# Kernel optimization log

Hardware: AMD Instinct MI355X
Metric: run time of the kernel (lower is better)

Reference implementation:

```python
import jax, jax.numpy as jnp
import numpy as np

RAD = 4   # corr lookup radius
NH, NP = 8, 4  # deform attn heads / points (single level)


def conv2d(x, w, b, pad):
    y = jax.lax.conv_general_dilated(x, w, (1, 1), [(pad, pad), (pad, pad)],
                                     dimension_numbers=('NCHW', 'OIHW', 'NCHW'))
    return y + b[None, :, None, None]


def bilinear_gather(imgf, H, W, px, py):
    # imgf: [N, C, H*W]; px, py: [N, P] pixel coords; zero padding (grid_sample 'zeros')
    x0 = jnp.floor(px); y0 = jnp.floor(py)
    wx = px - x0; wy = py - y0
    def tap(xi, yi, wt):
        valid = (xi >= 0) & (xi <= W - 1) & (yi >= 0) & (yi <= H - 1)
        idx = (jnp.clip(yi, 0, H - 1) * W + jnp.clip(xi, 0, W - 1)).astype(jnp.int32)
        v = jnp.take_along_axis(imgf, idx[:, None, :], axis=2)
        return v * (wt * valid)[:, None, :]
    return (tap(x0, y0, (1 - wx) * (1 - wy)) + tap(x0 + 1, y0, wx * (1 - wy))
            + tap(x0, y0 + 1, (1 - wx) * wy) + tap(x0 + 1, y0 + 1, wx * wy))


def sine_pos_embed(B, H, W, npf, temperature=10000.0):
    # PositionEmbeddingSine with normalize=True
    scale = 2.0 * np.pi; eps = 1e-6
    y = jnp.broadcast_to(jnp.arange(1, H + 1, dtype=jnp.float32)[:, None], (H, W))
    x = jnp.broadcast_to(jnp.arange(1, W + 1, dtype=jnp.float32)[None, :], (H, W))
    y = (y - 0.5) / (H + eps) * scale
    x = (x - 0.5) / (W + eps) * scale
    dim_t = temperature ** (2.0 * (jnp.arange(npf) // 2).astype(jnp.float32) / npf)
    px = x[..., None] / dim_t
    py = y[..., None] / dim_t
    px = jnp.stack([jnp.sin(px[..., 0::2]), jnp.cos(px[..., 1::2])], -1).reshape(H, W, npf)
    py = jnp.stack([jnp.sin(py[..., 0::2]), jnp.cos(py[..., 1::2])], -1).reshape(H, W, npf)
    pos = jnp.concatenate([py, px], -1)
    return jnp.broadcast_to(pos[None], (B, H, W, 2 * npf)).reshape(B, H * W, 2 * npf)


def layer_norm(x, g, b):
    m = x.mean(-1, keepdims=True)
    v = ((x - m) ** 2).mean(-1, keepdims=True)
    return (x - m) / jnp.sqrt(v + 1e-5) * g + b


def _forward(fmap1, fmap2, flow, wc1, bc1, wc2, bc2, wf1, bf1, wf2, bf2, wcf, bcf,
             wfh1, bfh1, wfh2, bfh2, w_off, b_off, w_aw, b_aw, w_val, b_val,
             w_out, b_out, ln1_g, ln1_b, w_ff1, b_ff1, w_ff2, b_ff2, ln2_g, ln2_b):
    B, C, H, W = fmap1.shape
    HW = H * W
    dh = C // NH
    relu = jax.nn.relu
    # ---- CorrBlock.corr: all-pairs correlation volume ----
    corr = jnp.einsum('bcq,bck->bqk', fmap1.reshape(B, C, HW), fmap2.reshape(B, C, HW))
    corr = corr / jnp.sqrt(jnp.asarray(C, jnp.float32))
    corrf = corr.reshape(B * HW, 1, HW)  # [B*HW, 1, H2*W2]
    # ---- correlation lookup at coords = base grid + flow (bilinear, align_corners=True) ----
    gy, gx = jnp.meshgrid(jnp.arange(H, dtype=jnp.float32),
                          jnp.arange(W, dtype=jnp.float32), indexing='ij')
    cx = (gx[None] + flow[:, 0]).reshape(B * HW)
    cy = (gy[None] + flow[:, 1]).reshape(B * HW)
    d = jnp.linspace(-RAD, RAD, 2 * RAD + 1)
    oy, ox = jnp.meshgrid(d, d, indexing='ij')  # RAFT quirk: delta[...,0]=dy, delta[...,1]=dx
    px = cx[:, None] + oy.reshape(-1)[None, :]
    py = cy[:, None] + ox.reshape(-1)[None, :]
    corr_feat = bilinear_gather(corrf, H, W, px, py).reshape(B, H, W, (2 * RAD + 1) ** 2)
    corr_feat = corr_feat.transpose(0, 3, 1, 2)  # [B, 81, H, W]
    # ---- BasicMotionEncoder + FlowHead (BasicUpdateBlock.forward path) ----
    cor = relu(conv2d(corr_feat, wc1, bc1, 0))
    cor = relu(conv2d(cor, wc2, bc2, 1))
    flo = relu(conv2d(flow, wf1, bf1, 3))
    flo = relu(conv2d(flo, wf2, bf2, 1))
    mf = relu(conv2d(jnp.concatenate([cor, flo], 1), wcf, bcf, 1))
    mf = jnp.concatenate([mf, flow], 1)  # [B,128,H,W]
    delta_flow = conv2d(relu(conv2d(mf, wfh1, bfh1, 1)), wfh2, bfh2, 1)  # [B,2,H,W]
    # ---- single-level MSDeformAttn encoder layer over fmap1 tokens ----
    src = fmap1.reshape(B, C, HW).transpose(0, 2, 1)  # [B, Lq, C]
    pos = sine_pos_embed(B, H, W, C // 2)
    q = src + pos
    off = (q @ w_off.T + b_off).reshape(B, HW, NH, 1, NP, 2)
    aw = jax.nn.softmax((q @ w_aw.T + b_aw).reshape(B, HW, NH, NP), axis=-1)
    val = (src @ w_val.T + b_val).reshape(B, HW, NH, dh)
    ref = jnp.stack([(gx.reshape(-1) + 0.5) / W, (gy.reshape(-1) + 0.5) / H], -1)  # [HW,2]
    loc = (ref[None, :, None, None, None, :] + off / jnp.asarray([W, H], jnp.float32))[:, :, :, 0]
    # normalized loc -> pixel coords with align_corners=False convention
    px2 = (loc[..., 0] * W - 0.5).transpose(0, 2, 1, 3).reshape(B * NH, HW * NP)
    py2 = (loc[..., 1] * H - 0.5).transpose(0, 2, 1, 3).reshape(B * NH, HW * NP)
    vflat = val.transpose(0, 2, 3, 1).reshape(B * NH, dh, HW)
    samp = bilinear_gather(vflat, H, W, px2, py2).reshape(B, NH, dh, HW, NP)
    attn = (samp * aw.transpose(0, 2, 1, 3)[:, :, None]).sum(-1)  # [B,NH,dh,HW]
    attn = attn.transpose(0, 3, 1, 2).reshape(B, HW, C) @ w_out.T + b_out
    src = layer_norm(src + attn, ln1_g, ln1_b)
    ff = jax.nn.relu(src @ w_ff1.T + b_ff1) @ w_ff2.T + b_ff2
    src = layer_norm(src + ff, ln2_g, ln2_b)
    return src, delta_flow


def setup_inputs():
    key = jax.random.key(0)
    ks = jax.random.split(key, 20)
    B, C, H, W = 4, 256, 48, 48
    def w(i, shape, s=0.02):
        return jax.random.normal(ks[i], shape, jnp.float32) * s
    return {
        'fmap1': jax.random.normal(ks[0], (B, C, H, W), jnp.float32),
        'fmap2': jax.random.normal(ks[1], (B, C, H, W), jnp.float32),
        'flow': jax.random.normal(ks[2], (B, 2, H, W), jnp.float32),
        'wc1': w(3, (256, 81, 1, 1)), 'bc1': jnp.zeros((256,)),
        'wc2': w(4, (192, 256, 3, 3)), 'bc2': jnp.zeros((192,)),
        'wf1': w(5, (128, 2, 7, 7)), 'bf1': jnp.zeros((128,)),
        'wf2': w(6, (64, 128, 3, 3)), 'bf2': jnp.zeros((64,)),
        'wcf': w(7, (126, 256, 3, 3)), 'bcf': jnp.zeros((126,)),
        'wfh1': w(8, (256, 128, 3, 3)), 'bfh1': jnp.zeros((256,)),
        'wfh2': w(9, (2, 256, 3, 3)), 'bfh2': jnp.zeros((2,)),
        'w_off': w(10, (64, 256)), 'b_off': jnp.zeros((64,)),
        'w_aw': w(11, (32, 256)), 'b_aw': jnp.zeros((32,)),
        'w_val': w(12, (256, 256)), 'b_val': jnp.zeros((256,)),
        'w_out': w(13, (256, 256)), 'b_out': jnp.zeros((256,)),
        'ln1_g': jnp.ones((256,)), 'ln1_b': jnp.zeros((256,)),
        'w_ff1': w(14, (1024, 256)), 'b_ff1': jnp.zeros((1024,)),
        'w_ff2': w(15, (256, 1024)), 'b_ff2': jnp.zeros((256,)),
        'ln2_g': jnp.ones((256,)), 'ln2_b': jnp.zeros((256,)),
    }


def reference(fmap1, fmap2, flow, wc1, bc1, wc2, bc2, wf1, bf1, wf2, bf2, wcf, bcf,
              wfh1, bfh1, wfh2, bfh2, w_off, b_off, w_aw, b_aw, w_val, b_val,
              w_out, b_out, ln1_g, ln1_b, w_ff1, b_ff1, w_ff2, b_ff2, ln2_g, ln2_b):
    return _forward(fmap1, fmap2, flow, wc1, bc1, wc2, bc2, wf1, bf1, wf2, bf2, wcf, bcf,
                    wfh1, bfh1, wfh2, bfh2, w_off, b_off, w_aw, b_aw, w_val, b_val,
                    w_out, b_out, ln1_g, ln1_b, w_ff1, b_ff1, w_ff2, b_ff2, ln2_g, ln2_b)
```

## Files before the change

kernel.cpp:

```cpp
#include <hip/hip_runtime.h>
#include <hip/hip_bf16.h>
#include <math.h>

#define HH 48
#define WW 48
#define HW 2304
#define BB 4
#define CC 256

typedef __hip_bfloat16 bf16;
typedef __attribute__((ext_vector_type(8))) short s8v;
typedef __attribute__((ext_vector_type(4))) float f4v;

__device__ inline float bf2f(short u) {
  unsigned v = ((unsigned)(unsigned short)u) << 16;
  return __builtin_bit_cast(float, v);
}

__global__ __launch_bounds__(256) void prep_k(const float* __restrict__ fmap1,
                                              const float* __restrict__ fmap2,
                                              float* __restrict__ srcT,
                                              bf16* __restrict__ f1t,
                                              bf16* __restrict__ qb,
                                              bf16* __restrict__ f2t) {
  __shared__ float t[64][65];
  int z = blockIdx.z;
  int p0 = blockIdx.x * 64, c0 = blockIdx.y * 64;
  int b = z & 3;
  const float* src = (z < 4) ? fmap2 : fmap1;
  const float* inb = src + ((size_t)b * CC + c0) * HW + p0;
#pragma unroll
  for (int i = 0; i < 16; ++i) {
    int idx = threadIdx.x + i * 256;
    int c = idx >> 6, p = idx & 63;
    t[c][p] = inb[(size_t)c * HW + p];
  }
  __syncthreads();
  if (z < 4) {
    bf16* ob = f2t + ((size_t)b * HW + p0) * 256 + c0;
#pragma unroll
    for (int i = 0; i < 16; ++i) {
      int idx = threadIdx.x + i * 256;
      int p = idx >> 6, c = idx & 63;
      ob[(size_t)p * 256 + c] = (bf16)t[c][p];
    }
  } else {
    const float TWO_PI = 6.283185307179586f;
#pragma unroll
    for (int i = 0; i < 16; ++i) {
      int idx = threadIdx.x + i * 256;
      int pl = idx >> 6, cl = idx & 63;
      int c = c0 + cl;
      int p = p0 + pl;
      int y = p / WW, x = p % WW;
      float s = t[cl][pl];
      int axis = c >> 7;
      int cc = c & 127;
      int mm = cc >> 1;
      float coord = (axis ? ((float)x + 0.5f) : ((float)y + 0.5f)) * (TWO_PI / (48.f + 1e-6f));
      float tp = exp2f((float)mm * (13.287712379549449f / 64.f));
      float a = coord / tp;
      float pv = (cc & 1) ? cosf(a) : sinf(a);
      size_t o = ((size_t)b * HW + p) * 256 + c;
      srcT[o] = s;
      f1t[o] = (bf16)s;
      qb[o] = (bf16)(s + pv);
    }
  }
}

__global__ __launch_bounds__(256) void corr_mfma_k(const bf16* __restrict__ f1t,
                                                   const bf16* __restrict__ f2t,
                                                   bf16* __restrict__ corr) {
  int b = blockIdx.z;
  int m0 = blockIdx.y * 128, n0 = blockIdx.x * 64;
  __shared__ short As[2][128][64];
  __shared__ short Bs[2][64][64];
  int tid = threadIdx.x;
  int arl = tid >> 1, asl = (tid & 1) * 4;
  int brl = tid >> 2, bsl = (tid & 3) * 2;
  int wave = tid >> 6, lane = tid & 63;
  int wm = (wave >> 1) * 64, wn = (wave & 1) * 32;
  int fl = lane & 15, fk8 = lane >> 4;
  f4v acc[4][2] = {};
  const bf16* arow = f1t + ((size_t)b * HW + m0 + arl) * 256;
  const bf16* brow = f2t + ((size_t)b * HW + n0 + brl) * 256;
  uint4 apre[4], bpre[2];
#pragma unroll
  for (int q = 0; q < 4; ++q) apre[q] = *(const uint4*)(arow + (asl + q) * 8);
#pragma unroll
  for (int q = 0; q < 2; ++q) bpre[q] = *(const uint4*)(brow + (bsl + q) * 8);
  int cur = 0;
  for (int st = 0; st < 4; ++st) {
#pragma unroll
    for (int q = 0; q < 4; ++q) {
      int sr = asl + q;
      *(uint4*)&As[cur][arl][((sr ^ (arl & 7))) * 8] = apre[q];
    }
#pragma unroll
    for (int q = 0; q < 2; ++q) {
      int sr = bsl + q;
      *(uint4*)&Bs[cur][brl][((sr ^ (brl & 7))) * 8] = bpre[q];
    }
    if (st < 3) {
      int c0 = (st + 1) * 64;
#pragma unroll
      for (int q = 0; q < 4; ++q) apre[q] = *(const uint4*)(arow + c0 + (asl + q) * 8);
#pragma unroll
      for (int q = 0; q < 2; ++q) bpre[q] = *(const uint4*)(brow + c0 + (bsl + q) * 8);
    }
    __syncthreads();
#pragma unroll
    for (int cc = 0; cc < 2; ++cc) {
      s8v af[4], bfr[2];
#pragma unroll
      for (int i = 0; i < 4; ++i) {
        int ar = wm + i * 16 + fl;
        af[i] = *(const s8v*)&As[cur][ar][(((cc * 4 + fk8) ^ (ar & 7))) * 8];
      }
#pragma unroll
      for (int j = 0; j < 2; ++j) {
        int br = wn + j * 16 + fl;
        bfr[j] = *(const s8v*)&Bs[cur][br][(((cc * 4 + fk8) ^ (br & 7))) * 8];
      }
#pragma unroll
      for (int i = 0; i < 4; ++i)
#pragma unroll
        for (int j = 0; j < 2; ++j)
          acc[i][j] = __builtin_amdgcn_mfma_f32_16x16x32_bf16(af[i], bfr[j], acc[i][j], 0, 0, 0);
    }
    cur ^= 1;
  }
  bf16* outp = corr + ((size_t)b * HW + m0) * HW + n0;
#pragma unroll
  for (int j = 0; j < 2; ++j) {
    int o = wn + j * 16 + fl;
#pragma unroll
    for (int i = 0; i < 4; ++i)
#pragma unroll
      for (int r = 0; r < 4; ++r) {
        int m = wm + i * 16 + fk8 * 4 + r;
        outp[(size_t)m * HW + o] = (bf16)(acc[i][j][r] * 0.0625f);
      }
  }
}

__global__ __launch_bounds__(256) void corr_lookup_k(const bf16* __restrict__ corr,
                                                     const float* __restrict__ flow,
                                                     bf16* __restrict__ cf) {
  int g = blockIdx.x * 256 + threadIdx.x;
  int t = g % 96;
  int n = g / 96;
  if (t >= 81) { cf[g] = (bf16)0.f; return; }
  int b = n / HW;
  int p = n % HW;
  int y = p / WW, x = p % WW;
  float fx = flow[((size_t)b * 2 + 0) * HW + p];
  float fy = flow[((size_t)b * 2 + 1) * HW + p];
  float px = (float)x + fx + (float)(t / 9 - 4);
  float py = (float)y + fy + (float)(t % 9 - 4);
  const bf16* row = corr + (size_t)n * HW;
  float x0f = floorf(px), y0f = floorf(py);
  int x0 = (int)x0f, y0 = (int)y0f;
  float wx = px - x0f, wy = py - y0f;
  float acc = 0.f;
  if ((unsigned)x0 < WW && (unsigned)y0 < HH) acc += (float)row[y0 * WW + x0] * (1.f - wx) * (1.f - wy);
  if ((unsigned)(x0 + 1) < WW && (unsigned)y0 < HH) acc += (float)row[y0 * WW + x0 + 1] * wx * (1.f - wy);
  if ((unsigned)x0 < WW && (unsigned)(y0 + 1) < HH) acc += (float)row[(y0 + 1) * WW + x0] * (1.f - wx) * wy;
  if ((unsigned)(x0 + 1) < WW && (unsigned)(y0 + 1) < HH) acc += (float)row[(y0 + 1) * WW + x0 + 1] * wx * wy;
  cf[g] = (bf16)acc;
}

struct WtSegs {
  const float* src[12];
  unsigned dstOff[12];
  int Cout[12], Cin[12], KP[12], KS2[12];
  unsigned cum[13];
};

__global__ __launch_bounds__(256) void wt_all_k(WtSegs s, bf16* __restrict__ base) {
  unsigned idx = blockIdx.x * 256 + threadIdx.x;
  if (idx >= s.cum[12]) return;
  int seg = 0;
#pragma unroll
  for (int i = 1; i < 12; ++i)
    if (idx >= s.cum[i]) seg = i;
  unsigned r = idx - s.cum[seg];
  int KP = s.KP[seg], Cout = s.Cout[seg], Cin = s.Cin[seg], KS2 = s.KS2[seg];
  int c = r % KP;
  int o = (r / KP) % Cout;
  int t = r / (KP * Cout);
  float v;
  if (KS2 == 0) {
    int cc = c >> 6, tt = c & 63;
    v = (tt < 49) ? s.src[seg][((size_t)o * 2 + cc) * 49 + tt] : 0.f;
  } else {
    v = (c < Cin) ? s.src[seg][((size_t)o * Cin + c) * KS2 + t] : 0.f;
  }
  base[s.dstOff[seg] + r] = (bf16)v;
}

__global__ __launch_bounds__(256) void im2col7_k(const float* __restrict__ flow,
                                                 bf16* __restrict__ col7) {
  int g = blockIdx.x * 256 + threadIdx.x;
  int kp = g & 127;
  int n = g >> 7;
  int b = n / HW;
  int p = n % HW;
  int y = p / WW, x = p % WW;
  int cc = kp >> 6, tt = kp & 63;
  float v = 0.f;
  if (tt < 49) {
    int ky = tt / 7, kx = tt % 7;
    int yy = y + ky - 3, xx = x + kx - 3;
    if ((unsigned)yy < (unsigned)HH && (unsigned)xx < (unsigned)WW)
      v = flow[((size_t)b * 2 + cc) * HW + yy * WW + xx];
  }
  col7[g] = (bf16)v;
}

struct GSegs {
  const bf16* in[4];
  const bf16* wt[4];
  const float* bias[4];
  const float* bias2[4];
  float* outf[4];
  bf16* outb[4];
  int split[4], O[4], KP[4], taps[4], OStride[4], OOff[4], relu[4], nTn[4];
  int blkStart[4];
  int nseg;
};

__global__ __launch_bounds__(256) void gemm_group_k(GSegs s) {
  int blk = blockIdx.x;
  int seg = 0;
#pragma unroll
  for (int i = 1; i < 4; ++i)
    if (i < s.nseg && blk >= s.blkStart[i]) seg = i;
  int rel = blk - s.blkStart[seg];
  int nTn = s.nTn[seg];
  int bm = rel / nTn, bn = rel % nTn;
  int m0 = bm * 128, n0 = bn * 64;
  int KP = s.KP[seg], O = s.O[seg], taps = s.taps[seg];
  const bf16* in = s.in[seg];
  const bf16* wt = s.wt[seg];

  __shared__ short As[2][128][64];
  __shared__ short Bs[2][64][64];
  int tid = threadIdx.x;
  int arl = tid >> 1, asl = (tid & 1) * 4;
  int brl = tid >> 2, bsl = (tid & 3) * 2;
  int wave = tid >> 6, lane = tid & 63;
  int wm = (wave >> 1) * 64, wn = (wave & 1) * 32;
  int fl = lane & 15, fk8 = lane >> 4;
  f4v acc[4][2] = {};
  int m = m0 + arl;
  int b = m / HW;
  int p = m - b * HW;
  int y = p / WW, x = p - y * WW;
  int wo = n0 + brl;
  bool wvalid = wo < O;
  int wo_c = wvalid ? wo : 0;

  int nc0 = (KP + 63) >> 6;
  int S = taps * nc0;
  uint4 apre[4], bpre[2];

  auto load_stage = [&](int st) {
    int t = st / nc0;
    int c0 = (st - t * nc0) * 64;
    int yy = y, xx = x;
    bool valid = true;
    if (taps == 9) {
      int ky = t / 3, kx = t - ky * 3;
      yy = y + ky - 1;
      xx = x + kx - 1;
      valid = ((unsigned)yy < (unsigned)HH) & ((unsigned)xx < (unsigned)WW);
    }
    const bf16* arow = in + ((size_t)b * HW + yy * WW + xx) * KP;
    const bf16* wrow = wt + ((size_t)t * O + wo_c) * KP;
#pragma unroll
    for (int q = 0; q < 4; ++q) {
      int col = c0 + (asl + q) * 8;
      uint4 v = {0u, 0u, 0u, 0u};
      if (valid && col < KP) v = *(const uint4*)(arow + col);
      apre[q] = v;
    }
#pragma unroll
    for (int q = 0; q < 2; ++q) {
      int col = c0 + (bsl + q) * 8;
      uint4 v = {0u, 0u, 0u, 0u};
      if (wvalid && col < KP) v = *(const uint4*)(wrow + col);
      bpre[q] = v;
    }
  };

  load_stage(0);
  int cur = 0;
  for (int st = 0; st < S; ++st) {
#pragma unroll
    for (int q = 0; q < 4; ++q) {
      int sr = asl + q;
      *(uint4*)&As[cur][arl][((sr ^ (arl & 7))) * 8] = apre[q];
    }
#pragma unroll
    for (int q = 0; q < 2; ++q) {
      int sr = bsl + q;
      *(uint4*)&Bs[cur][brl][((sr ^ (brl & 7))) * 8] = bpre[q];
    }
    if (st + 1 < S) load_stage(st + 1);
    __syncthreads();
#pragma unroll
    for (int cc = 0; cc < 2; ++cc) {
      s8v af[4], bfr[2];
#pragma unroll
      for (int i = 0; i < 4; ++i) {
        int ar = wm + i * 16 + fl;
        af[i] = *(const s8v*)&As[cur][ar][(((cc * 4 + fk8) ^ (ar & 7))) * 8];
      }
#pragma unroll
      for (int j = 0; j < 2; ++j) {
        int br = wn + j * 16 + fl;
        bfr[j] = *(const s8v*)&Bs[cur][br][(((cc * 4 + fk8) ^ (br & 7))) * 8];
      }
#pragma unroll
      for (int i = 0; i < 4; ++i)
#pragma unroll
        for (int j = 0; j < 2; ++j)
          acc[i][j] = __builtin_amdgcn_mfma_f32_16x16x32_bf16(af[i], bfr[j], acc[i][j], 0, 0, 0);
    }
    cur ^= 1;
  }
  int OStride = s.OStride[seg], OOff = s.OOff[seg], relu = s.relu[seg], split = s.split[seg];
  const float* bias = s.bias[seg];
  const float* bias2 = s.bias2[seg];
  float* outf = s.outf[seg];
  bf16* outb = s.outb[seg];
#pragma unroll
  for (int j = 0; j < 2; ++j) {
    int o = n0 + wn + j * 16 + fl;
    if (o < O) {
      float bsv = (bias2 != nullptr && o >= split) ? bias2[o - split] : bias[o];
#pragma unroll
      for (int i = 0; i < 4; ++i)
#pragma unroll
        for (int r = 0; r < 4; ++r) {
          int mm = m0 + wm + i * 16 + fk8 * 4 + r;
          float v = acc[i][j][r] + bsv;
          if (relu) v = fmaxf(v, 0.f);
          if (outb) outb[(size_t)mm * OStride + OOff + o] = (bf16)v;
          else outf[(size_t)mm * OStride + OOff + o] = v;
        }
    }
  }
}

__global__ __launch_bounds__(256) void convfh2_k(const bf16* __restrict__ fh1,
                                                 const float* __restrict__ w,
                                                 const float* __restrict__ bias,
                                                 float* __restrict__ out) {
  __shared__ float wl[4608];
  int tid = threadIdx.x;
#pragma unroll
  for (int i = tid; i < 4608; i += 256) {
    int o2 = i & 1;
    int t = (i >> 1) % 9;
    int c = i / 18;
    wl[i] = w[((size_t)o2 * 256 + c) * 9 + t];
  }
  __syncthreads();
  int wave = tid >> 6, lane = tid & 63;
  int pix = blockIdx.x * 4 + wave;
  int b = pix / HW;
  int q = pix % HW;
  int y = q / WW, x = q % WW;
  int c0 = lane * 4;
  float a0 = 0.f, a1 = 0.f;
#pragma unroll
  for (int ky = 0; ky < 3; ++ky) {
    int yy = y + ky - 1;
    if ((unsigned)yy >= (unsigned)HH) continue;
#pragma unroll
    for (int kx = 0; kx < 3; ++kx) {
      int xx = x + kx - 1;
      if ((unsigned)xx >= (unsigned)WW) continue;
      int t = ky * 3 + kx;
      const bf16* row = fh1 + ((size_t)b * HW + yy * WW + xx) * 256 + c0;
      ushort4 v = *(const ushort4*)row;
      unsigned short vv[4] = {v.x, v.y, v.z, v.w};
#pragma unroll
      for (int j = 0; j < 4; ++j) {
        float fv = bf2f((short)vv[j]);
        float2 wp = *(const float2*)&wl[((c0 + j) * 9 + t) * 2];
        a0 += fv * wp.x;
        a1 += fv * wp.y;
      }
    }
  }
#pragma unroll
  for (int offl = 32; offl > 0; offl >>= 1) {
    a0 += __shfl_xor(a0, offl);
    a1 += __shfl_xor(a1, offl);
  }
  if (lane == 0) {
    out[(size_t)b * 2 * HW + q] = a0 + bias[0];
    out[((size_t)b * 2 + 1) * HW + q] = a1 + bias[1];
  }
}

__global__ void copy_flow_k(const float* __restrict__ flow, bf16* __restrict__ mf) {
  int g = blockIdx.x * 256 + threadIdx.x;
  int p = g % HW;
  int c = (g / HW) % 2;
  int b = g / (2 * HW);
  mf[((size_t)b * HW + p) * 128 + 126 + c] = (bf16)flow[g];
}

__global__ __launch_bounds__(256) void deform_k(const float* __restrict__ val,
                                                const float* __restrict__ oa,
                                                bf16* __restrict__ attn) {
  int g = blockIdx.x * 256 + threadIdx.x;
  int d = g & 31;
  int nh = g >> 5;
  int h = nh & 7;
  int n = nh >> 3;
  int b = n / HW;
  int p = n % HW;
  int y = p / WW, x = p % WW;
  const float* ap = oa + (size_t)n * 96 + 64 + h * 4;
  float l0 = ap[0], l1 = ap[1], l2 = ap[2], l3 = ap[3];
  float mx = fmaxf(fmaxf(l0, l1), fmaxf(l2, l3));
  float e0 = expf(l0 - mx), e1 = expf(l1 - mx), e2 = expf(l2 - mx), e3 = expf(l3 - mx);
  float inv = 1.f / (e0 + e1 + e2 + e3);
  float wts[4] = {e0 * inv, e1 * inv, e2 * inv, e3 * inv};
  const float* offp = oa + (size_t)n * 96 + h * 8;
  const float* vb = val + (size_t)b * HW * 256 + h * 32 + d;
  float acc = 0.f;
#pragma unroll
  for (int pt = 0; pt < 4; ++pt) {
    float ox = offp[pt * 2 + 0];
    float oy = offp[pt * 2 + 1];
    float w = wts[pt];
    float px = (float)x + ox, py = (float)y + oy;
    float x0f = floorf(px), y0f = floorf(py);
    int x0 = (int)x0f, y0 = (int)y0f;
    float wx = px - x0f, wy = py - y0f;
    float s = 0.f;
    if ((unsigned)x0 < WW && (unsigned)y0 < HH)
      s += vb[(size_t)(y0 * WW + x0) * 256] * (1.f - wx) * (1.f - wy);
    if ((unsigned)(x0 + 1) < WW && (unsigned)y0 < HH)
      s += vb[(size_t)(y0 * WW + x0 + 1) * 256] * wx * (1.f - wy);
    if ((unsigned)x0 < WW && (unsigned)(y0 + 1) < HH)
      s += vb[(size_t)((y0 + 1) * WW + x0) * 256] * (1.f - wx) * wy;
    if ((unsigned)(x0 + 1) < WW && (unsigned)(y0 + 1) < HH)
      s += vb[(size_t)((y0 + 1) * WW + x0 + 1) * 256] * wx * wy;
    acc += w * s;
  }
  attn[(size_t)n * 256 + h * 32 + d] = (bf16)acc;
}

__global__ __launch_bounds__(256) void ln_add_k(const float* __restrict__ A,
                                                const float* __restrict__ Bv,
                                                const float* __restrict__ g,
                                                const float* __restrict__ be,
                                                float* __restrict__ out,
                                                bf16* __restrict__ outb) {
  int n = blockIdx.x;
  int c = threadIdx.x;
  float v = A[(size_t)n * 256 + c] + Bv[(size_t)n * 256 + c];
  float s1 = v, s2 = v * v;
#pragma unroll
  for (int o = 32; o > 0; o >>= 1) {
    s1 += __shfl_down(s1, o);
    s2 += __shfl_down(s2, o);
  }
  __shared__ float r1[4], r2[4], mv[2];
  int wid = c >> 6, lane = c & 63;
  if (lane == 0) {
    r1[wid] = s1;
    r2[wid] = s2;
  }
  __syncthreads();
  if (c == 0) {
    float a = r1[0] + r1[1] + r1[2] + r1[3];
    float q2 = r2[0] + r2[1] + r2[2] + r2[3];
    float mean = a * (1.f / 256.f);
    mv[0] = mean;
    mv[1] = q2 * (1.f / 256.f) - mean * mean;
  }
  __syncthreads();
  float mean = mv[0], var = mv[1];
  float r = (v - mean) * rsqrtf(var + 1e-5f) * g[c] + be[c];
  out[(size_t)n * 256 + c] = r;
  if (outb) outb[(size_t)n * 256 + c] = (bf16)r;
}

extern "C" void kernel_launch(void* const* d_in, const int* in_sizes, int n_in,
                              void* d_out, int out_size, void* d_ws, size_t ws_size,
                              hipStream_t stream) {
  const float* fmap1 = (const float*)d_in[0];
  const float* fmap2 = (const float*)d_in[1];
  const float* flow = (const float*)d_in[2];
  const float* wc1 = (const float*)d_in[3];
  const float* bc1 = (const float*)d_in[4];
  const float* wc2 = (const float*)d_in[5];
  const float* bc2 = (const float*)d_in[6];
  const float* wf1 = (const float*)d_in[7];
  const float* bf1 = (const float*)d_in[8];
  const float* wf2 = (const float*)d_in[9];
  const float* bf2 = (const float*)d_in[10];
  const float* wcf = (const float*)d_in[11];
  const float* bcf = (const float*)d_in[12];
  const float* wfh1 = (const float*)d_in[13];
  const float* bfh1 = (const float*)d_in[14];
  const float* wfh2 = (const float*)d_in[15];
  const float* bfh2 = (const float*)d_in[16];
  const float* w_off = (const float*)d_in[17];
  const float* b_off = (const float*)d_in[18];
  const float* w_aw = (const float*)d_in[19];
  const float* b_aw = (const float*)d_in[20];
  const float* w_val = (const float*)d_in[21];
  const float* b_val = (const float*)d_in[22];
  const float* w_out = (const float*)d_in[23];
  const float* b_out = (const float*)d_in[24];
  const float* ln1_g = (const float*)d_in[25];
  const float* ln1_b = (const float*)d_in[26];
  const float* w_ff1 = (const float*)d_in[27];
  const float* b_ff1 = (const float*)d_in[28];
  const float* w_ff2 = (const float*)d_in[29];
  const float* b_ff2 = (const float*)d_in[30];
  const float* ln2_g = (const float*)d_in[31];
  const float* ln2_b = (const float*)d_in[32];

  float* ws = (float*)d_ws;
  float* out_src = (float*)d_out;
  float* out_df = out_src + (size_t)BB * HW * CC;

  const size_t F_WT = 0;
  const size_t F_CORR = 1000000;
  const size_t F_F1T = 11700000;
  const size_t F_F2T = 12900000;
  const size_t F_QB = 14100000;
  const size_t F_SRCT = 15300000;
  const size_t F_CF = 17700000;
  const size_t F_COL7 = 18200000;
  const size_t F_COR1 = 18800000;
  const size_t F_FLO1 = 20000000;
  const size_t F_CAT = 20600000;
  const size_t F_MF = 21800000;
  const size_t F_FH1 = 22400000;
  const size_t F_OA = 23600000;
  const size_t F_VAL = 24500000;
  const size_t F_ATTN = 26900000;
  const size_t F_TMP = 28100000;
  const size_t F_SRC1 = 30500000;
  const size_t F_SRC1B = 32900000;
  const size_t F_FF1 = 34100000;
  const size_t F_FF2 = 38900000;

  bf16* wkbase = (bf16*)(ws + F_WT);
  bf16* wk1 = wkbase + 0;
  bf16* wk2 = wkbase + 24576;
  bf16* wkf2 = wkbase + 466944;
  bf16* wkcf = wkbase + 540672;
  bf16* wkfh1 = wkbase + 830976;
  bf16* wl_oa = wkbase + 1125888;
  bf16* wl_val = wkbase + 1150464;
  bf16* wl_out = wkbase + 1216000;
  bf16* wl_ff1 = wkbase + 1281536;
  bf16* wl_ff2 = wkbase + 1543680;
  bf16* wk7 = wkbase + 1805824;
  bf16* corrb = (bf16*)(ws + F_CORR);
  bf16* f1t = (bf16*)(ws + F_F1T);
  bf16* f2t = (bf16*)(ws + F_F2T);
  bf16* qb = (bf16*)(ws + F_QB);
  bf16* cf = (bf16*)(ws + F_CF);
  bf16* col7 = (bf16*)(ws + F_COL7);
  bf16* cor1 = (bf16*)(ws + F_COR1);
  bf16* flo1 = (bf16*)(ws + F_FLO1);
  bf16* cat = (bf16*)(ws + F_CAT);
  bf16* mf = (bf16*)(ws + F_MF);
  bf16* fh1 = (bf16*)(ws + F_FH1);
  bf16* attnb = (bf16*)(ws + F_ATTN);
  bf16* src1b = (bf16*)(ws + F_SRC1B);
  bf16* ff1b = (bf16*)(ws + F_FF1);

  WtSegs segs;
  const float* srcs[12] = {wc1, wc2, wf2, wcf, wfh1, w_off, w_aw, w_val, w_out, w_ff1, w_ff2, wf1};
  unsigned offs[12] = {0, 24576, 466944, 540672, 830976, 1125888, 1142272, 1150464, 1216000, 1281536, 1543680, 1805824};
  int couts[12] = {256, 192, 64, 126, 256, 64, 32, 256, 256, 1024, 256, 128};
  int cins[12] = {81, 256, 128, 256, 128, 256, 256, 256, 256, 256, 1024, 2};
  int kps[12] = {96, 256, 128, 256, 128, 256, 256, 256, 256, 256, 1024, 128};
  int ks2[12] = {1, 9, 9, 9, 9, 1, 1, 1, 1, 1, 1, 0};
  unsigned cum = 0;
  for (int i = 0; i < 12; ++i) {
    segs.src[i] = srcs[i];
    segs.dstOff[i] = offs[i];
    segs.Cout[i] = couts[i];
    segs.Cin[i] = cins[i];
    segs.KP[i] = kps[i];
    segs.KS2[i] = ks2[i];
    segs.cum[i] = cum;
    cum += (unsigned)((ks2[i] ? ks2[i] : 1) * couts[i] * kps[i]);
  }
  segs.cum[12] = cum;
  wt_all_k<<<dim3((cum + 255) / 256), 256, 0, stream>>>(segs, wkbase);

  prep_k<<<dim3(36, 4, 8), 256, 0, stream>>>(fmap1, fmap2, ws + F_SRCT, f1t, qb, f2t);
  im2col7_k<<<dim3(4608), 256, 0, stream>>>(flow, col7);
  copy_flow_k<<<dim3(72), 256, 0, stream>>>(flow, mf);

  corr_mfma_k<<<dim3(36, 18, 4), 256, 0, stream>>>(f1t, f2t, corrb);
  corr_lookup_k<<<dim3(3456), 256, 0, stream>>>(corrb, flow, cf);

  auto setseg = [](GSegs& G, int i, const bf16* in, const bf16* wt, const float* bias,
                   const float* bias2, int split, float* outf, bf16* outb, int O, int KP,
                   int taps, int OStride, int OOff, int relu) {
    G.in[i] = in; G.wt[i] = wt; G.bias[i] = bias; G.bias2[i] = bias2; G.split[i] = split;
    G.outf[i] = outf; G.outb[i] = outb; G.O[i] = O; G.KP[i] = KP; G.taps[i] = taps;
    G.OStride[i] = OStride; G.OOff[i] = OOff; G.relu[i] = relu;
    G.nTn[i] = (O + 63) / 64;
  };
  auto finseg = [](GSegs& G, int n) {
    int cumb = 0;
    for (int i = 0; i < 4; ++i) {
      if (i < n) { G.blkStart[i] = cumb; cumb += G.nTn[i] * 72; }
      else G.blkStart[i] = 0x7fffffff;
    }
    G.nseg = n;
    return cumb;
  };

  GSegs GA;
  setseg(GA, 0, cf, wk1, bc1, nullptr, 1 << 30, nullptr, cor1, 256, 96, 1, 256, 0, 1);
  setseg(GA, 1, col7, wk7, bf1, nullptr, 1 << 30, nullptr, flo1, 128, 128, 1, 128, 0, 1);
  setseg(GA, 2, qb, wl_oa, b_off, b_aw, 64, ws + F_OA, nullptr, 96, 256, 1, 96, 0, 0);
  setseg(GA, 3, f1t, wl_val, b_val, nullptr, 1 << 30, ws + F_VAL, nullptr, 256, 256, 1, 256, 0, 0);
  int nblkA = finseg(GA, 4);
  gemm_group_k<<<dim3(nblkA), 256, 0, stream>>>(GA);

  deform_k<<<dim3(9216), 256, 0, stream>>>(ws + F_VAL, ws + F_OA, attnb);

  GSegs GB;
  setseg(GB, 0, cor1, wk2, bc2, nullptr, 1 << 30, nullptr, cat, 192, 256, 9, 256, 0, 1);
  setseg(GB, 1, flo1, wkf2, bf2, nullptr, 1 << 30, nullptr, cat, 64, 128, 9, 256, 192, 1);
  setseg(GB, 2, attnb, wl_out, b_out, nullptr, 1 << 30, ws + F_TMP, nullptr, 256, 256, 1, 256, 0, 0);
  int nblkB = finseg(GB, 3);
  gemm_group_k<<<dim3(nblkB), 256, 0, stream>>>(GB);

  ln_add_k<<<dim3(9216), 256, 0, stream>>>(ws + F_TMP, ws + F_SRCT, ln1_g, ln1_b, ws + F_SRC1, src1b);

  GSegs GC;
  setseg(GC, 0, cat, wkcf, bcf, nullptr, 1 << 30, nullptr, mf, 126, 256, 9, 128, 0, 1);
  setseg(GC, 1, src1b, wl_ff1, b_ff1, nullptr, 1 << 30, nullptr, ff1b, 1024, 256, 1, 1024, 0, 1);
  int nblkC = finseg(GC, 2);
  gemm_group_k<<<dim3(nblkC), 256, 0, stream>>>(GC);

  GSegs GD;
  setseg(GD, 0, mf, wkfh1, bfh1, nullptr, 1 << 30, nullptr, fh1, 256, 128, 9, 256, 0, 1);
  setseg(GD, 1, ff1b, wl_ff2, b_ff2, nullptr, 1 << 30, ws + F_FF2, nullptr, 256, 1024, 1, 256, 0, 0);
  int nblkD = finseg(GD, 2);
  gemm_group_k<<<dim3(nblkD), 256, 0, stream>>>(GD);

  convfh2_k<<<dim3(2304), 256, 0, stream>>>(fh1, wfh2, bfh2, out_df);
  ln_add_k<<<dim3(9216), 256, 0, stream>>>(ws + F_FF2, ws + F_SRC1, ln2_g, ln2_b, out_src, nullptr);

  (void)in_sizes; (void)n_in; (void)out_size; (void)ws_size;
}
```

Baseline: 286.0 us.

## Fuse correlation and lookup into local-window dot products per pixel

Replaces the all-pairs MFMA correlation volume and the separate bilinear lookup kernel with one kernel. For each pixel it computes dot products only for the 10x10 integer window around the flow target, then bilinearly interpolates the 9x9 taps from that shared window. The goal is to skip the full HWxHW matmul and the large bf16 correlation buffer write and read. In exchange the dot products run as scalar FMAs with gathered f2t rows instead of on matrix cores, and corr values are no longer rounded to bf16 before interpolation.

```diff
diff --git a/kernel.cpp b/kernel.cpp
--- a/kernel.cpp
+++ b/kernel.cpp
@@ -69,106 +69,71 @@
   }
 }
 
-__global__ __launch_bounds__(256) void corr_mfma_k(const bf16* __restrict__ f1t,
-                                                   const bf16* __restrict__ f2t,
-                                                   bf16* __restrict__ corr) {
-  int b = blockIdx.z;
-  int m0 = blockIdx.y * 128, n0 = blockIdx.x * 64;
-  __shared__ short As[2][128][64];
-  __shared__ short Bs[2][64][64];
-  int tid = threadIdx.x;
-  int arl = tid >> 1, asl = (tid & 1) * 4;
-  int brl = tid >> 2, bsl = (tid & 3) * 2;
-  int wave = tid >> 6, lane = tid & 63;
-  int wm = (wave >> 1) * 64, wn = (wave & 1) * 32;
-  int fl = lane & 15, fk8 = lane >> 4;
-  f4v acc[4][2] = {};
-  const bf16* arow = f1t + ((size_t)b * HW + m0 + arl) * 256;
-  const bf16* brow = f2t + ((size_t)b * HW + n0 + brl) * 256;
-  uint4 apre[4], bpre[2];
-#pragma unroll
-  for (int q = 0; q < 4; ++q) apre[q] = *(const uint4*)(arow + (asl + q) * 8);
-#pragma unroll
-  for (int q = 0; q < 2; ++q) bpre[q] = *(const uint4*)(brow + (bsl + q) * 8);
-  int cur = 0;
-  for (int st = 0; st < 4; ++st) {
-#pragma unroll
-    for (int q = 0; q < 4; ++q) {
-      int sr = asl + q;
-      *(uint4*)&As[cur][arl][((sr ^ (arl & 7))) * 8] = apre[q];
-    }
-#pragma unroll
-    for (int q = 0; q < 2; ++q) {
-      int sr = bsl + q;
-      *(uint4*)&Bs[cur][brl][((sr ^ (brl & 7))) * 8] = bpre[q];
-    }
-    if (st < 3) {
-      int c0 = (st + 1) * 64;
-#pragma unroll
-      for (int q = 0; q < 4; ++q) apre[q] = *(const uint4*)(arow + c0 + (asl + q) * 8);
-#pragma unroll
-      for (int q = 0; q < 2; ++q) bpre[q] = *(const uint4*)(brow + c0 + (bsl + q) * 8);
-    }
-    __syncthreads();
-#pragma unroll
-    for (int cc = 0; cc < 2; ++cc) {
-      s8v af[4], bfr[2];
-#pragma unroll
-      for (int i = 0; i < 4; ++i) {
-        int ar = wm + i * 16 + fl;
-        af[i] = *(const s8v*)&As[cur][ar][(((cc * 4 + fk8) ^ (ar & 7))) * 8];
-      }
-#pragma unroll
-      for (int j = 0; j < 2; ++j) {
-        int br = wn + j * 16 + fl;
-        bfr[j] = *(const s8v*)&Bs[cur][br][(((cc * 4 + fk8) ^ (br & 7))) * 8];
-      }
-#pragma unroll
-      for (int i = 0; i < 4; ++i)
-#pragma unroll
-        for (int j = 0; j < 2; ++j)
-          acc[i][j] = __builtin_amdgcn_mfma_f32_16x16x32_bf16(af[i], bfr[j], acc[i][j], 0, 0, 0);
-    }
-    cur ^= 1;
-  }
-  bf16* outp = corr + ((size_t)b * HW + m0) * HW + n0;
-#pragma unroll
-  for (int j = 0; j < 2; ++j) {
-    int o = wn + j * 16 + fl;
-#pragma unroll
-    for (int i = 0; i < 4; ++i)
-#pragma unroll
-      for (int r = 0; r < 4; ++r) {
-        int m = wm + i * 16 + fk8 * 4 + r;
-        outp[(size_t)m * HW + o] = (bf16)(acc[i][j][r] * 0.0625f);
-      }
-  }
-}
-
-__global__ __launch_bounds__(256) void corr_lookup_k(const bf16* __restrict__ corr,
-                                                     const float* __restrict__ flow,
-                                                     bf16* __restrict__ cf) {
-  int g = blockIdx.x * 256 + threadIdx.x;
-  int t = g % 96;
-  int n = g / 96;
-  if (t >= 81) { cf[g] = (bf16)0.f; return; }
-  int b = n / HW;
-  int p = n % HW;
-  int y = p / WW, x = p % WW;
+__global__ __launch_bounds__(256) void fused_corr_k(const bf16* __restrict__ f1t,
+                                                    const bf16* __restrict__ f2t,
+                                                    const float* __restrict__ flow,
+                                                    bf16* __restrict__ cf) {
+  __shared__ float f1s[4][260];
+  __shared__ float Dls[4][112];
+  int wave = threadIdx.x >> 6, lane = threadIdx.x & 63;
+  int q = blockIdx.x * 4 + wave;
+  int b = q / HW, p = q - b * HW;
+  int y = p / WW, x = p - y * WW;
+  {
+    ushort4 v = *(const ushort4*)(f1t + (size_t)q * 256 + lane * 4);
+    f1s[wave][lane * 4 + 0] = bf2f((short)v.x);
+    f1s[wave][lane * 4 + 1] = bf2f((short)v.y);
+    f1s[wave][lane * 4 + 2] = bf2f((short)v.z);
+    f1s[wave][lane * 4 + 3] = bf2f((short)v.w);
+  }
   float fx = flow[((size_t)b * 2 + 0) * HW + p];
   float fy = flow[((size_t)b * 2 + 1) * HW + p];
-  float px = (float)x + fx + (float)(t / 9 - 4);
-  float py = (float)y + fy + (float)(t % 9 - 4);
-  const bf16* row = corr + (size_t)n * HW;
-  float x0f = floorf(px), y0f = floorf(py);
-  int x0 = (int)x0f, y0 = (int)y0f;
-  float wx = px - x0f, wy = py - y0f;
-  float acc = 0.f;
-  if ((unsigned)x0 < WW && (unsigned)y0 < HH) acc += (float)row[y0 * WW + x0] * (1.f - wx) * (1.f - wy);
-  if ((unsigned)(x0 + 1) < WW && (unsigned)y0 < HH) acc += (float)row[y0 * WW + x0 + 1] * wx * (1.f - wy);
-  if ((unsigned)x0 < WW && (unsigned)(y0 + 1) < HH) acc += (float)row[(y0 + 1) * WW + x0] * (1.f - wx) * wy;
-  if ((unsigned)(x0 + 1) < WW && (unsigned)(y0 + 1) < HH) acc += (float)row[(y0 + 1) * WW + x0 + 1] * wx * wy;
-  cf[g] = (bf16)acc;
+  float sx = (float)x + fx, sy = (float)y + fy;
+  float fx0 = floorf(sx), fy0 = floorf(sy);
+  int ix0 = (int)fx0, iy0 = (int)fy0;
+  float wx = sx - fx0, wy = sy - fy0;
+  __syncthreads();
+  const float* f1p = f1s[wave];
+#pragma unroll
+  for (int r = 0; r < 2; ++r) {
+    int idx = lane + r * 64;
+    if (idx < 100) {
+      int jy = idx / 10, jx = idx - jy * 10;
+      int ky = iy0 - 4 + jy, kx = ix0 - 4 + jx;
+      float acc = 0.f;
+      if ((unsigned)kx < (unsigned)WW && (unsigned)ky < (unsigned)HH) {
+        const bf16* row = f2t + ((size_t)b * HW + ky * WW + kx) * 256;
+#pragma unroll
+        for (int c8 = 0; c8 < 32; ++c8) {
+          uint4 v = *(const uint4*)(row + c8 * 8);
+          int c = c8 * 8;
+          acc += bf2f((short)(v.x & 0xffff)) * f1p[c + 0];
+          acc += bf2f((short)(v.x >> 16)) * f1p[c + 1];
+          acc += bf2f((short)(v.y & 0xffff)) * f1p[c + 2];
+          acc += bf2f((short)(v.y >> 16)) * f1p[c + 3];
+          acc += bf2f((short)(v.z & 0xffff)) * f1p[c + 4];
+          acc += bf2f((short)(v.z >> 16)) * f1p[c + 5];
+          acc += bf2f((short)(v.w & 0xffff)) * f1p[c + 6];
+          acc += bf2f((short)(v.w >> 16)) * f1p[c + 7];
+        }
+      }
+      Dls[wave][idx] = acc * 0.0625f;
+    }
+  }
+  __syncthreads();
+  float w00 = (1.f - wx) * (1.f - wy), w10 = wx * (1.f - wy);
+  float w01 = (1.f - wx) * wy, w11 = wx * wy;
+  const float* D = Dls[wave];
+  bf16* cfr = cf + (size_t)q * 96;
+  for (int t = lane; t < 96; t += 64) {
+    float v = 0.f;
+    if (t < 81) {
+      int jx = t / 9, jy = t - jx * 9;
+      v = w00 * D[jy * 10 + jx] + w10 * D[jy * 10 + jx + 1] +
+          w01 * D[(jy + 1) * 10 + jx] + w11 * D[(jy + 1) * 10 + jx + 1];
+    }
+    cfr[t] = (bf16)v;
+  }
 }
 
 struct WtSegs {
@@ -537,7 +502,6 @@
   float* out_df = out_src + (size_t)BB * HW * CC;
 
   const size_t F_WT = 0;
-  const size_t F_CORR = 1000000;
   const size_t F_F1T = 11700000;
   const size_t F_F2T = 12900000;
   const size_t F_QB = 14100000;
@@ -570,7 +534,6 @@
   bf16* wl_ff1 = wkbase + 1281536;
   bf16* wl_ff2 = wkbase + 1543680;
   bf16* wk7 = wkbase + 1805824;
-  bf16* corrb = (bf16*)(ws + F_CORR);
   bf16* f1t = (bf16*)(ws + F_F1T);
   bf16* f2t = (bf16*)(ws + F_F2T);
   bf16* qb = (bf16*)(ws + F_QB);
@@ -610,8 +573,7 @@
   im2col7_k<<<dim3(4608), 256, 0, stream>>>(flow, col7);
   copy_flow_k<<<dim3(72), 256, 0, stream>>>(flow, mf);
 
-  corr_mfma_k<<<dim3(36, 18, 4), 256, 0, stream>>>(f1t, f2t, corrb);
-  corr_lookup_k<<<dim3(3456), 256, 0, stream>>>(corrb, flow, cf);
+  fused_corr_k<<<dim3(2304), 256, 0, stream>>>(f1t, f2t, flow, cf);
 
   auto setseg = [](GSegs& G, int i, const bf16* in, const bf16* wt, const float* bias,
                    const float* bias2, int split, float* outf, bf16* outb, int O, int KP,
```

Result: faster. 278.5 us (-2.6%).
